# Performance work log

Measured on AMD Instinct MI355X. Metric: run time of the kernel, lower is better.

The kernel has to match this reference:

```python
import jax, jax.numpy as jnp
import numpy as np

IN_FEATURES = 1024
OUT_FEATURES = 1024
B, S = 8, 4096


def setup_inputs() -> dict:
    key = jax.random.key(0)
    kx, kw = jax.random.split(key)
    x = jax.random.normal(kx, (B, S, IN_FEATURES), dtype=jnp.float32)
    # weight initialized as randn * 0.1, shape [out_features, in_features]
    weight = jax.random.normal(kw, (OUT_FEATURES, IN_FEATURES), dtype=jnp.float32) * 0.1
    bias = jnp.zeros((OUT_FEATURES,), dtype=jnp.float32)
    return {"x": x, "weight": weight, "bias": bias}


def reference(x, weight, bias):
    # BitNetLinear eval-mode forward.
    # Weight quantization to ternary {-1, 0, +1} with mean-abs scale.
    w_scale = jnp.mean(jnp.abs(weight))  # scalar
    q_weight = jnp.sign(weight) * (jnp.abs(weight) > 0.5 * w_scale).astype(weight.dtype)
    # Activation quantization to int8 range with global abs-max scale.
    i_scale = jnp.max(jnp.abs(x)) / 127.0  # scalar
    q_input = jnp.clip(jnp.round(x / i_scale), -128.0, 127.0)
    # Float GEMM on quantized values, then dequant with both scales.
    out = jnp.einsum('bsk,ok->bso', q_input, q_weight) * w_scale * i_scale
    out = out + bias  # bias added after dequant, matching the torch code
    return out
```

## Files before the change

### kernel.cpp

```cpp
#include <hip/hip_runtime.h>
#include <stdint.h>


#define MK_M 32768
#define MK_K 1024
#define MK_N 1024

typedef __attribute__((ext_vector_type(4))) int int32x4;

#define WS_MAXP_OFF 64
#define WS_PART_OFF 8448
#define WS_QW_OFF 16384
#define WS_QX_OFF (16384 + (1 << 20))
#define WS_NEEDED (WS_QX_OFF + (size_t)MK_M * MK_K)

__global__ void kmax_x(const float4* __restrict__ x4, float* __restrict__ maxp, long n4) {
    float m = 0.f;
    long stride = (long)gridDim.x * blockDim.x;
    for (long i = (long)blockIdx.x * blockDim.x + threadIdx.x; i < n4; i += stride) {
        float4 v = x4[i];
        m = fmaxf(m, fmaxf(fmaxf(fabsf(v.x), fabsf(v.y)), fmaxf(fabsf(v.z), fabsf(v.w))));
    }
    #pragma unroll
    for (int off = 1; off < 64; off <<= 1) m = fmaxf(m, __shfl_xor(m, off));
    __shared__ float sm[4];
    int lane = threadIdx.x & 63, wid = threadIdx.x >> 6;
    if (lane == 0) sm[wid] = m;
    __syncthreads();
    if (threadIdx.x == 0) maxp[blockIdx.x] = fmaxf(fmaxf(sm[0], sm[1]), fmaxf(sm[2], sm[3]));
}

__global__ void ksum_w(const float4* __restrict__ w4, double* __restrict__ partials) {
    double s = 0.0;
    for (int i = blockIdx.x * 256 + threadIdx.x; i < (1 << 18); i += 256 * 256) {
        float4 v = w4[i];
        s += (double)fabsf(v.x);
        s += (double)fabsf(v.y);
        s += (double)fabsf(v.z);
        s += (double)fabsf(v.w);
    }
    __shared__ double sd[256];
    sd[threadIdx.x] = s;
    __syncthreads();
    for (int h = 128; h > 0; h >>= 1) {
        if ((int)threadIdx.x < h) sd[threadIdx.x] += sd[threadIdx.x + h];
        __syncthreads();
    }
    if (threadIdx.x == 0) partials[blockIdx.x] = sd[0];
}

__global__ void kfin(const double* __restrict__ partials, const float* __restrict__ maxp,
                     float* __restrict__ wscp, float* __restrict__ iscp) {
    int t = threadIdx.x;
    float m = 0.f;
    #pragma unroll
    for (int j = 0; j < 32; ++j) m = fmaxf(m, maxp[t + 64 * j]);
    double s = partials[4 * t] + partials[4 * t + 1] + partials[4 * t + 2] + partials[4 * t + 3];
    #pragma unroll
    for (int off = 1; off < 64; off <<= 1) {
        m = fmaxf(m, __shfl_xor(m, off));
        s = s + __shfl_xor(s, off);
    }
    if (t == 0) {
        *wscp = (float)(s / 1048576.0);
        *iscp = m / 127.0f;
    }
}

__global__ void kquant_w(const float4* __restrict__ w4, unsigned* __restrict__ qw,
                         const float* __restrict__ wscp) {
    float thr = 0.5f * (*wscp);
    int stride = gridDim.x * blockDim.x;
    for (int i = blockIdx.x * blockDim.x + threadIdx.x; i < (1 << 18); i += stride) {
        float4 v = w4[i];
        int q0 = (fabsf(v.x) > thr) ? (v.x > 0.f ? 1 : -1) : 0;
        int q1 = (fabsf(v.y) > thr) ? (v.y > 0.f ? 1 : -1) : 0;
        int q2 = (fabsf(v.z) > thr) ? (v.z > 0.f ? 1 : -1) : 0;
        int q3 = (fabsf(v.w) > thr) ? (v.w > 0.f ? 1 : -1) : 0;
        qw[i] = (q0 & 0xff) | ((q1 & 0xff) << 8) | ((q2 & 0xff) << 16) | ((q3 & 0xff) << 24);
    }
}

__global__ void kquant_x(const float4* __restrict__ x4, unsigned* __restrict__ qx,
                         const float* __restrict__ iscp, long n4) {
    float isc = *iscp;
    long stride = (long)gridDim.x * blockDim.x;
    for (long i = (long)blockIdx.x * blockDim.x + threadIdx.x; i < n4; i += stride) {
        float4 v = x4[i];
        float q0 = fminf(fmaxf(rintf(v.x / isc), -128.f), 127.f);
        float q1 = fminf(fmaxf(rintf(v.y / isc), -128.f), 127.f);
        float q2 = fminf(fmaxf(rintf(v.z / isc), -128.f), 127.f);
        float q3 = fminf(fmaxf(rintf(v.w / isc), -128.f), 127.f);
        int i0 = (int)q0, i1 = (int)q1, i2 = (int)q2, i3 = (int)q3;
        qx[i] = (i0 & 0xff) | ((i1 & 0xff) << 8) | ((i2 & 0xff) << 16) | ((i3 & 0xff) << 24);
    }
}

__global__ __launch_bounds__(512, 2) void kgemm(
    const char* __restrict__ qx, const char* __restrict__ qw,
    const float* __restrict__ bias, const float* __restrict__ wscp,
    const float* __restrict__ iscp, float* __restrict__ out)
{
    __shared__ __align__(16) char smem[3 * 32768];

    const int t = threadIdx.x;
    const int l = t & 63;
    const int w = t >> 6;
    const int wm = w >> 2;
    const int wn = w & 3;

    const int bid = blockIdx.x;
    const int wg = (bid & 7) * 64 + (bid >> 3);
    const int tm = wg >> 2, tn = wg & 3;
    const long m0 = (long)tm * 256;
    const int n0 = tn * 256;

    const int grow = t >> 2;
    const int gch = (t & 3) ^ ((t >> 3) & 3);
    const long goff = (long)grow * MK_K + gch * 16;
    const int loff = t * 16;

    const char* gAt = qx + m0 * MK_K + goff;
    const char* gBt = qw + (long)n0 * MK_K + goff;

    int32x4 acc[8][4];
    #pragma unroll
    for (int mi = 0; mi < 8; ++mi)
        #pragma unroll
        for (int ni = 0; ni < 4; ++ni) acc[mi][ni] = (int32x4)0;

    auto stage = [&](int u, int kt, int b) {
        char* nbase = smem + b * 32768;
        const char* src;
        char* dst;
        if (u < 2) {
            src = gAt + (long)u * 128 * MK_K + kt * 64;
            dst = nbase + u * 8192 + loff;
        } else {
            src = gBt + (long)(u - 2) * 128 * MK_K + kt * 64;
            dst = nbase + 16384 + (u - 2) * 8192 + loff;
        }
        __builtin_amdgcn_global_load_lds(
            (const __attribute__((address_space(1))) void*)src,
            (__attribute__((address_space(3))) void*)dst, 16, 0, 0);
    };

    #pragma unroll
    for (int u = 0; u < 4; ++u) stage(u, 0, 0);
    #pragma unroll
    for (int u = 0; u < 4; ++u) stage(u, 1, 1);

    for (int kt = 0; kt < 16; ++kt) {
        if (kt < 15) asm volatile("s_waitcnt vmcnt(4)" ::: "memory");
        else         asm volatile("s_waitcnt vmcnt(0)" ::: "memory");
        __builtin_amdgcn_s_barrier();

        const int cb = kt % 3;
        const int nb = (kt + 2) % 3;
        const char* bufA = smem + cb * 32768;
        const char* bufB = bufA + 16384;

        int32x4 af[8], bf[4];
        #pragma unroll
        for (int i = 0; i < 8; ++i) {
            int row = wm * 128 + i * 16 + (l & 15);
            int ch = (l >> 4) ^ ((row >> 1) & 3);
            af[i] = *(const int32x4*)(bufA + row * 64 + ch * 16);
        }
        #pragma unroll
        for (int i = 0; i < 4; ++i) {
            int row = wn * 64 + i * 16 + (l & 15);
            int ch = (l >> 4) ^ ((row >> 1) & 3);
            bf[i] = *(const int32x4*)(bufB + row * 64 + ch * 16);
        }
        if (kt < 14) {
            #pragma unroll
            for (int u = 0; u < 4; ++u) stage(u, kt + 2, nb);
        }
        __builtin_amdgcn_s_setprio(1);
        #pragma unroll
        for (int mi = 0; mi < 8; ++mi)
            #pragma unroll
            for (int ni = 0; ni < 4; ++ni)
                acc[mi][ni] = __builtin_amdgcn_mfma_i32_16x16x64_i8(
                    af[mi], bf[ni], acc[mi][ni], 0, 0, 0);
        __builtin_amdgcn_s_setprio(0);
    }

    const float wsc = *wscp, isc = *iscp;
    const int crow = (l >> 4) * 4;
    const int ccol = l & 15;
    #pragma unroll
    for (int mi = 0; mi < 8; ++mi) {
        #pragma unroll
        for (int ni = 0; ni < 4; ++ni) {
            long r0 = m0 + wm * 128 + mi * 16 + crow;
            int c = n0 + wn * 64 + ni * 16 + ccol;
            float b = bias[c];
            #pragma unroll
            for (int j = 0; j < 4; ++j) {
                out[(r0 + j) * MK_N + c] = ((float)acc[mi][ni][j] * wsc) * isc + b;
            }
        }
    }
}

extern "C" void kernel_launch(void* const* d_in, const int* in_sizes, int n_in,
                              void* d_out, int out_size, void* d_ws, size_t ws_size,
                              hipStream_t stream) {
    const float* x = (const float*)d_in[0];
    const float* wt = (const float*)d_in[1];
    const float* bias = (const float*)d_in[2];
    float* out = (float*)d_out;

    if (ws_size < WS_NEEDED) return;

    char* ws = (char*)d_ws;
    float* wscp = (float*)(ws + 0);
    float* iscp = (float*)(ws + 4);
    float* maxp = (float*)(ws + WS_MAXP_OFF);
    double* partials = (double*)(ws + WS_PART_OFF);
    char* qw = ws + WS_QW_OFF;
    char* qx = ws + WS_QX_OFF;

    const long n_x = (long)in_sizes[0];
    const long n4_x = n_x >> 2;

    kmax_x<<<2048, 256, 0, stream>>>((const float4*)x, maxp, n4_x);
    ksum_w<<<256, 256, 0, stream>>>((const float4*)wt, partials);
    kfin<<<1, 64, 0, stream>>>(partials, maxp, wscp, iscp);
    kquant_w<<<256, 256, 0, stream>>>((const float4*)wt, (unsigned*)qw, wscp);
    kquant_x<<<2048, 256, 0, stream>>>((const float4*)x, (unsigned*)qx, iscp, n4_x);

    const int grid = (MK_M / 256) * (MK_N / 256);
    kgemm<<<grid, 512, 0, stream>>>(qx, qw, bias, wscp, iscp, out);
}
```

Baseline: 109.9 us.

## Merge prep kernels and load GEMM B fragments directly from global memory

Merges the x abs-max and weight abs-sum reductions into one launch. The final reduction moves into the quantize kernels, so five pre-GEMM launches become three. The GEMM no longer stages the weight tile in LDS: each wave loads its B fragments straight from global memory into registers with inline asm, double-buffered across k-steps. The A buffer goes from triple to double buffering, which reduces LDS use. The risk is that direct global loads of B are less coalesced, rely on cache reuse across waves, and add register pressure.

```diff
diff --git a/kernel.cpp b/kernel.cpp
--- a/kernel.cpp
+++ b/kernel.cpp
@@ -14,62 +14,56 @@
 #define WS_QX_OFF (16384 + (1 << 20))
 #define WS_NEEDED (WS_QX_OFF + (size_t)MK_M * MK_K)
 
-__global__ void kmax_x(const float4* __restrict__ x4, float* __restrict__ maxp, long n4) {
-    float m = 0.f;
-    long stride = (long)gridDim.x * blockDim.x;
-    for (long i = (long)blockIdx.x * blockDim.x + threadIdx.x; i < n4; i += stride) {
-        float4 v = x4[i];
-        m = fmaxf(m, fmaxf(fmaxf(fabsf(v.x), fabsf(v.y)), fmaxf(fabsf(v.z), fabsf(v.w))));
-    }
-    #pragma unroll
-    for (int off = 1; off < 64; off <<= 1) m = fmaxf(m, __shfl_xor(m, off));
-    __shared__ float sm[4];
-    int lane = threadIdx.x & 63, wid = threadIdx.x >> 6;
-    if (lane == 0) sm[wid] = m;
+__global__ void kprep(const float4* __restrict__ x4, const float4* __restrict__ w4,
+                      float* __restrict__ maxp, double* __restrict__ partials, long n4x) {
+    const int bid = blockIdx.x;
+    if (bid < 2048) {
+        float m = 0.f;
+        const long stride = 2048L * 256;
+        for (long i = (long)bid * 256 + threadIdx.x; i < n4x; i += stride) {
+            float4 v = x4[i];
+            m = fmaxf(m, fmaxf(fmaxf(fabsf(v.x), fabsf(v.y)), fmaxf(fabsf(v.z), fabsf(v.w))));
+        }
+        #pragma unroll
+        for (int off = 1; off < 64; off <<= 1) m = fmaxf(m, __shfl_xor(m, off));
+        __shared__ float sm[4];
+        int lane = threadIdx.x & 63, wid = threadIdx.x >> 6;
+        if (lane == 0) sm[wid] = m;
+        __syncthreads();
+        if (threadIdx.x == 0) maxp[bid] = fmaxf(fmaxf(sm[0], sm[1]), fmaxf(sm[2], sm[3]));
+    } else {
+        double s = 0.0;
+        for (int i = (bid - 2048) * 256 + threadIdx.x; i < (1 << 18); i += 64 * 256) {
+            float4 v = w4[i];
+            s += (double)fabsf(v.x);
+            s += (double)fabsf(v.y);
+            s += (double)fabsf(v.z);
+            s += (double)fabsf(v.w);
+        }
+        __shared__ double sd[256];
+        sd[threadIdx.x] = s;
+        __syncthreads();
+        for (int h = 128; h > 0; h >>= 1) {
+            if ((int)threadIdx.x < h) sd[threadIdx.x] += sd[threadIdx.x + h];
+            __syncthreads();
+        }
+        if (threadIdx.x == 0) partials[bid - 2048] = sd[0];
+    }
+}
+
+__global__ void kquant_w(const float4* __restrict__ w4, unsigned* __restrict__ qw,
+                         const double* __restrict__ partials, float* __restrict__ wscp) {
+    __shared__ double sws;
+    if (threadIdx.x < 64) {
+        double s = partials[threadIdx.x];
+        #pragma unroll
+        for (int off = 1; off < 64; off <<= 1) s += __shfl_xor(s, off);
+        if (threadIdx.x == 0) sws = s;
+    }
     __syncthreads();
-    if (threadIdx.x == 0) maxp[blockIdx.x] = fmaxf(fmaxf(sm[0], sm[1]), fmaxf(sm[2], sm[3]));
-}
-
-__global__ void ksum_w(const float4* __restrict__ w4, double* __restrict__ partials) {
-    double s = 0.0;
-    for (int i = blockIdx.x * 256 + threadIdx.x; i < (1 << 18); i += 256 * 256) {
-        float4 v = w4[i];
-        s += (double)fabsf(v.x);
-        s += (double)fabsf(v.y);
-        s += (double)fabsf(v.z);
-        s += (double)fabsf(v.w);
-    }
-    __shared__ double sd[256];
-    sd[threadIdx.x] = s;
-    __syncthreads();
-    for (int h = 128; h > 0; h >>= 1) {
-        if ((int)threadIdx.x < h) sd[threadIdx.x] += sd[threadIdx.x + h];
-        __syncthreads();
-    }
-    if (threadIdx.x == 0) partials[blockIdx.x] = sd[0];
-}
-
-__global__ void kfin(const double* __restrict__ partials, const float* __restrict__ maxp,
-                     float* __restrict__ wscp, float* __restrict__ iscp) {
-    int t = threadIdx.x;
-    float m = 0.f;
-    #pragma unroll
-    for (int j = 0; j < 32; ++j) m = fmaxf(m, maxp[t + 64 * j]);
-    double s = partials[4 * t] + partials[4 * t + 1] + partials[4 * t + 2] + partials[4 * t + 3];
-    #pragma unroll
-    for (int off = 1; off < 64; off <<= 1) {
-        m = fmaxf(m, __shfl_xor(m, off));
-        s = s + __shfl_xor(s, off);
-    }
-    if (t == 0) {
-        *wscp = (float)(s / 1048576.0);
-        *iscp = m / 127.0f;
-    }
-}
-
-__global__ void kquant_w(const float4* __restrict__ w4, unsigned* __restrict__ qw,
-                         const float* __restrict__ wscp) {
-    float thr = 0.5f * (*wscp);
+    float wsc = (float)(sws / 1048576.0);
+    if (blockIdx.x == 0 && threadIdx.x == 0) *wscp = wsc;
+    float thr = 0.5f * wsc;
     int stride = gridDim.x * blockDim.x;
     for (int i = blockIdx.x * blockDim.x + threadIdx.x; i < (1 << 18); i += stride) {
         float4 v = w4[i];
@@ -82,8 +76,18 @@
 }
 
 __global__ void kquant_x(const float4* __restrict__ x4, unsigned* __restrict__ qx,
-                         const float* __restrict__ iscp, long n4) {
-    float isc = *iscp;
+                         const float* __restrict__ maxp, float* __restrict__ iscp, long n4) {
+    float m = 0.f;
+    #pragma unroll
+    for (int j = 0; j < 8; ++j) m = fmaxf(m, maxp[threadIdx.x + 256 * j]);
+    #pragma unroll
+    for (int off = 1; off < 64; off <<= 1) m = fmaxf(m, __shfl_xor(m, off));
+    __shared__ float sm[4];
+    int lane = threadIdx.x & 63, wid = threadIdx.x >> 6;
+    if (lane == 0) sm[wid] = m;
+    __syncthreads();
+    float isc = fmaxf(fmaxf(sm[0], sm[1]), fmaxf(sm[2], sm[3])) / 127.0f;
+    if (blockIdx.x == 0 && threadIdx.x == 0) *iscp = isc;
     long stride = (long)gridDim.x * blockDim.x;
     for (long i = (long)blockIdx.x * blockDim.x + threadIdx.x; i < n4; i += stride) {
         float4 v = x4[i];
@@ -101,7 +105,7 @@
     const float* __restrict__ bias, const float* __restrict__ wscp,
     const float* __restrict__ iscp, float* __restrict__ out)
 {
-    __shared__ __align__(16) char smem[3 * 32768];
+    __shared__ __align__(16) char smem[2 * 16384];
 
     const int t = threadIdx.x;
     const int l = t & 63;
@@ -116,75 +120,80 @@
     const int n0 = tn * 256;
 
     const int grow = t >> 2;
-    const int gch = (t & 3) ^ ((t >> 3) & 3);
-    const long goff = (long)grow * MK_K + gch * 16;
-    const int loff = t * 16;
-
-    const char* gAt = qx + m0 * MK_K + goff;
-    const char* gBt = qw + (long)n0 * MK_K + goff;
-
-    int32x4 acc[8][4];
-    #pragma unroll
-    for (int mi = 0; mi < 8; ++mi)
-        #pragma unroll
-        for (int ni = 0; ni < 4; ++ni) acc[mi][ni] = (int32x4)0;
-
-    auto stage = [&](int u, int kt, int b) {
-        char* nbase = smem + b * 32768;
-        const char* src;
-        char* dst;
-        if (u < 2) {
-            src = gAt + (long)u * 128 * MK_K + kt * 64;
-            dst = nbase + u * 8192 + loff;
-        } else {
-            src = gBt + (long)(u - 2) * 128 * MK_K + kt * 64;
-            dst = nbase + 16384 + (u - 2) * 8192 + loff;
-        }
+    const int gch = (t & 3) ^ ((grow >> 1) & 3);
+    const char* gAt = qx + (m0 + grow) * (long)MK_K + gch * 16;
+
+    auto stage = [&](int kt1, int b) {
+        char* dst = smem + b * 16384 + t * 16;
+        const char* src = gAt + kt1 * 64;
         __builtin_amdgcn_global_load_lds(
             (const __attribute__((address_space(1))) void*)src,
             (__attribute__((address_space(3))) void*)dst, 16, 0, 0);
+        __builtin_amdgcn_global_load_lds(
+            (const __attribute__((address_space(1))) void*)(src + 128 * (long)MK_K),
+            (__attribute__((address_space(3))) void*)(dst + 8192), 16, 0, 0);
     };
 
-    #pragma unroll
-    for (int u = 0; u < 4; ++u) stage(u, 0, 0);
-    #pragma unroll
-    for (int u = 0; u < 4; ++u) stage(u, 1, 1);
-
-    for (int kt = 0; kt < 16; ++kt) {
-        if (kt < 15) asm volatile("s_waitcnt vmcnt(4)" ::: "memory");
-        else         asm volatile("s_waitcnt vmcnt(0)" ::: "memory");
+    const unsigned vo0 = (unsigned)((n0 + wn * 64 + 0 * 16 + (l & 15)) * MK_K + (l >> 4) * 16);
+    const unsigned vo1 = vo0 + 16 * MK_K;
+    const unsigned vo2 = vo0 + 32 * MK_K;
+    const unsigned vo3 = vo0 + 48 * MK_K;
+
+    int32x4 acc[8][4];
+    #pragma unroll
+    for (int mi = 0; mi < 8; ++mi)
+        #pragma unroll
+        for (int ni = 0; ni < 4; ++ni) acc[mi][ni] = (int32x4)0;
+
+    int32x4 bfA[4], bfB[4];
+
+    stage(0, 0);
+    {
+        const char* sb = qw;
+        asm volatile("global_load_dwordx4 %0, %1, %2" : "=v"(bfA[0]) : "v"(vo0), "s"(sb));
+        asm volatile("global_load_dwordx4 %0, %1, %2" : "=v"(bfA[1]) : "v"(vo1), "s"(sb));
+        asm volatile("global_load_dwordx4 %0, %1, %2" : "=v"(bfA[2]) : "v"(vo2), "s"(sb));
+        asm volatile("global_load_dwordx4 %0, %1, %2" : "=v"(bfA[3]) : "v"(vo3), "s"(sb));
+    }
+
+    auto body = [&](int kt, int32x4 (&bfc)[4], int32x4 (&bfn)[4]) {
+        asm volatile("s_waitcnt vmcnt(4)" ::: "memory");
         __builtin_amdgcn_s_barrier();
-
-        const int cb = kt % 3;
-        const int nb = (kt + 2) % 3;
-        const char* bufA = smem + cb * 32768;
-        const char* bufB = bufA + 16384;
-
-        int32x4 af[8], bf[4];
+        __builtin_amdgcn_sched_barrier(0);
+
+        const char* bufA = smem + (kt & 1) * 16384;
+        int32x4 af[8];
         #pragma unroll
         for (int i = 0; i < 8; ++i) {
             int row = wm * 128 + i * 16 + (l & 15);
             int ch = (l >> 4) ^ ((row >> 1) & 3);
             af[i] = *(const int32x4*)(bufA + row * 64 + ch * 16);
         }
-        #pragma unroll
-        for (int i = 0; i < 4; ++i) {
-            int row = wn * 64 + i * 16 + (l & 15);
-            int ch = (l >> 4) ^ ((row >> 1) & 3);
-            bf[i] = *(const int32x4*)(bufB + row * 64 + ch * 16);
-        }
-        if (kt < 14) {
-            #pragma unroll
-            for (int u = 0; u < 4; ++u) stage(u, kt + 2, nb);
-        }
+        if (kt < 15) {
+            stage(kt + 1, (kt + 1) & 1);
+            const char* sb = qw + (kt + 1) * 64;
+            asm volatile("global_load_dwordx4 %0, %1, %2" : "=v"(bfn[0]) : "v"(vo0), "s"(sb));
+            asm volatile("global_load_dwordx4 %0, %1, %2" : "=v"(bfn[1]) : "v"(vo1), "s"(sb));
+            asm volatile("global_load_dwordx4 %0, %1, %2" : "=v"(bfn[2]) : "v"(vo2), "s"(sb));
+            asm volatile("global_load_dwordx4 %0, %1, %2" : "=v"(bfn[3]) : "v"(vo3), "s"(sb));
+            asm volatile("s_waitcnt vmcnt(6) lgkmcnt(0)" ::: "memory");
+        } else {
+            asm volatile("s_waitcnt vmcnt(0) lgkmcnt(0)" ::: "memory");
+        }
+        __builtin_amdgcn_sched_barrier(0);
         __builtin_amdgcn_s_setprio(1);
         #pragma unroll
         for (int mi = 0; mi < 8; ++mi)
             #pragma unroll
             for (int ni = 0; ni < 4; ++ni)
                 acc[mi][ni] = __builtin_amdgcn_mfma_i32_16x16x64_i8(
-                    af[mi], bf[ni], acc[mi][ni], 0, 0, 0);
+                    af[mi], bfc[ni], acc[mi][ni], 0, 0, 0);
         __builtin_amdgcn_s_setprio(0);
+    };
+
+    for (int kb = 0; kb < 8; ++kb) {
+        body(2 * kb,     bfA, bfB);
+        body(2 * kb + 1, bfB, bfA);
     }
 
     const float wsc = *wscp, isc = *iscp;
@@ -226,11 +235,9 @@
     const long n_x = (long)in_sizes[0];
     const long n4_x = n_x >> 2;
 
-    kmax_x<<<2048, 256, 0, stream>>>((const float4*)x, maxp, n4_x);
-    ksum_w<<<256, 256, 0, stream>>>((const float4*)wt, partials);
-    kfin<<<1, 64, 0, stream>>>(partials, maxp, wscp, iscp);
-    kquant_w<<<256, 256, 0, stream>>>((const float4*)wt, (unsigned*)qw, wscp);
-    kquant_x<<<2048, 256, 0, stream>>>((const float4*)x, (unsigned*)qx, iscp, n4_x);
+    kprep<<<2112, 256, 0, stream>>>((const float4*)x, (const float4*)wt, maxp, partials, n4_x);
+    kquant_w<<<256, 256, 0, stream>>>((const float4*)wt, (unsigned*)qw, partials, wscp);
+    kquant_x<<<2048, 256, 0, stream>>>((const float4*)x, (unsigned*)qx, maxp, iscp, n4_x);
 
     const int grid = (MK_M / 256) * (MK_N / 256);
     kgemm<<<grid, 512, 0, stream>>>(qx, qw, bias, wscp, iscp, out);
```

New measurement: 120.2 us. +9.4%, slower.

## Merge prep reductions into fewer launches and split GEMM k-step into two phases

Applied to the files above, without the earlier changes.

Combines the x abs-max and weight abs-sum reductions into one kernel and folds the final scale reductions into the quantize kernels, which drops two launches and the single-block finalize kernel. Each quantize block now re-reduces the partials redundantly. In the GEMM, each k-tile is split into two half-phases that interleave LDS fragment loads, global-to-LDS staging and MFMAs, with extra barriers between them. This lowers register pressure for fragments but adds synchronization per k-step.

```diff
diff --git a/kernel.cpp b/kernel.cpp
--- a/kernel.cpp
+++ b/kernel.cpp
@@ -14,62 +14,56 @@
 #define WS_QX_OFF (16384 + (1 << 20))
 #define WS_NEEDED (WS_QX_OFF + (size_t)MK_M * MK_K)
 
-__global__ void kmax_x(const float4* __restrict__ x4, float* __restrict__ maxp, long n4) {
-    float m = 0.f;
-    long stride = (long)gridDim.x * blockDim.x;
-    for (long i = (long)blockIdx.x * blockDim.x + threadIdx.x; i < n4; i += stride) {
-        float4 v = x4[i];
-        m = fmaxf(m, fmaxf(fmaxf(fabsf(v.x), fabsf(v.y)), fmaxf(fabsf(v.z), fabsf(v.w))));
-    }
-    #pragma unroll
-    for (int off = 1; off < 64; off <<= 1) m = fmaxf(m, __shfl_xor(m, off));
-    __shared__ float sm[4];
-    int lane = threadIdx.x & 63, wid = threadIdx.x >> 6;
-    if (lane == 0) sm[wid] = m;
+__global__ void kprep(const float4* __restrict__ x4, const float4* __restrict__ w4,
+                      float* __restrict__ maxp, double* __restrict__ partials, long n4x) {
+    const int bid = blockIdx.x;
+    if (bid < 2048) {
+        float m = 0.f;
+        const long stride = 2048L * 256;
+        for (long i = (long)bid * 256 + threadIdx.x; i < n4x; i += stride) {
+            float4 v = x4[i];
+            m = fmaxf(m, fmaxf(fmaxf(fabsf(v.x), fabsf(v.y)), fmaxf(fabsf(v.z), fabsf(v.w))));
+        }
+        #pragma unroll
+        for (int off = 1; off < 64; off <<= 1) m = fmaxf(m, __shfl_xor(m, off));
+        __shared__ float sm[4];
+        int lane = threadIdx.x & 63, wid = threadIdx.x >> 6;
+        if (lane == 0) sm[wid] = m;
+        __syncthreads();
+        if (threadIdx.x == 0) maxp[bid] = fmaxf(fmaxf(sm[0], sm[1]), fmaxf(sm[2], sm[3]));
+    } else {
+        double s = 0.0;
+        for (int i = (bid - 2048) * 256 + threadIdx.x; i < (1 << 18); i += 64 * 256) {
+            float4 v = w4[i];
+            s += (double)fabsf(v.x);
+            s += (double)fabsf(v.y);
+            s += (double)fabsf(v.z);
+            s += (double)fabsf(v.w);
+        }
+        __shared__ double sd[256];
+        sd[threadIdx.x] = s;
+        __syncthreads();
+        for (int h = 128; h > 0; h >>= 1) {
+            if ((int)threadIdx.x < h) sd[threadIdx.x] += sd[threadIdx.x + h];
+            __syncthreads();
+        }
+        if (threadIdx.x == 0) partials[bid - 2048] = sd[0];
+    }
+}
+
+__global__ void kquant_w(const float4* __restrict__ w4, unsigned* __restrict__ qw,
+                         const double* __restrict__ partials, float* __restrict__ wscp) {
+    __shared__ double sws;
+    if (threadIdx.x < 64) {
+        double s = partials[threadIdx.x];
+        #pragma unroll
+        for (int off = 1; off < 64; off <<= 1) s += __shfl_xor(s, off);
+        if (threadIdx.x == 0) sws = s;
+    }
     __syncthreads();
-    if (threadIdx.x == 0) maxp[blockIdx.x] = fmaxf(fmaxf(sm[0], sm[1]), fmaxf(sm[2], sm[3]));
-}
-
-__global__ void ksum_w(const float4* __restrict__ w4, double* __restrict__ partials) {
-    double s = 0.0;
-    for (int i = blockIdx.x * 256 + threadIdx.x; i < (1 << 18); i += 256 * 256) {
-        float4 v = w4[i];
-        s += (double)fabsf(v.x);
-        s += (double)fabsf(v.y);
-        s += (double)fabsf(v.z);
-        s += (double)fabsf(v.w);
-    }
-    __shared__ double sd[256];
-    sd[threadIdx.x] = s;
-    __syncthreads();
-    for (int h = 128; h > 0; h >>= 1) {
-        if ((int)threadIdx.x < h) sd[threadIdx.x] += sd[threadIdx.x + h];
-        __syncthreads();
-    }
-    if (threadIdx.x == 0) partials[blockIdx.x] = sd[0];
-}
-
-__global__ void kfin(const double* __restrict__ partials, const float* __restrict__ maxp,
-                     float* __restrict__ wscp, float* __restrict__ iscp) {
-    int t = threadIdx.x;
-    float m = 0.f;
-    #pragma unroll
-    for (int j = 0; j < 32; ++j) m = fmaxf(m, maxp[t + 64 * j]);
-    double s = partials[4 * t] + partials[4 * t + 1] + partials[4 * t + 2] + partials[4 * t + 3];
-    #pragma unroll
-    for (int off = 1; off < 64; off <<= 1) {
-        m = fmaxf(m, __shfl_xor(m, off));
-        s = s + __shfl_xor(s, off);
-    }
-    if (t == 0) {
-        *wscp = (float)(s / 1048576.0);
-        *iscp = m / 127.0f;
-    }
-}
-
-__global__ void kquant_w(const float4* __restrict__ w4, unsigned* __restrict__ qw,
-                         const float* __restrict__ wscp) {
-    float thr = 0.5f * (*wscp);
+    float wsc = (float)(sws / 1048576.0);
+    if (blockIdx.x == 0 && threadIdx.x == 0) *wscp = wsc;
+    float thr = 0.5f * wsc;
     int stride = gridDim.x * blockDim.x;
     for (int i = blockIdx.x * blockDim.x + threadIdx.x; i < (1 << 18); i += stride) {
         float4 v = w4[i];
@@ -82,8 +76,18 @@
 }
 
 __global__ void kquant_x(const float4* __restrict__ x4, unsigned* __restrict__ qx,
-                         const float* __restrict__ iscp, long n4) {
-    float isc = *iscp;
+                         const float* __restrict__ maxp, float* __restrict__ iscp, long n4) {
+    float m = 0.f;
+    #pragma unroll
+    for (int j = 0; j < 8; ++j) m = fmaxf(m, maxp[threadIdx.x + 256 * j]);
+    #pragma unroll
+    for (int off = 1; off < 64; off <<= 1) m = fmaxf(m, __shfl_xor(m, off));
+    __shared__ float sm[4];
+    int lane = threadIdx.x & 63, wid = threadIdx.x >> 6;
+    if (lane == 0) sm[wid] = m;
+    __syncthreads();
+    float isc = fmaxf(fmaxf(sm[0], sm[1]), fmaxf(sm[2], sm[3])) / 127.0f;
+    if (blockIdx.x == 0 && threadIdx.x == 0) *iscp = isc;
     long stride = (long)gridDim.x * blockDim.x;
     for (long i = (long)blockIdx.x * blockDim.x + threadIdx.x; i < n4; i += stride) {
         float4 v = x4[i];
@@ -159,32 +163,38 @@
         const int nb = (kt + 2) % 3;
         const char* bufA = smem + cb * 32768;
         const char* bufB = bufA + 16384;
-
-        int32x4 af[8], bf[4];
-        #pragma unroll
-        for (int i = 0; i < 8; ++i) {
-            int row = wm * 128 + i * 16 + (l & 15);
-            int ch = (l >> 4) ^ ((row >> 1) & 3);
-            af[i] = *(const int32x4*)(bufA + row * 64 + ch * 16);
-        }
-        #pragma unroll
-        for (int i = 0; i < 4; ++i) {
-            int row = wn * 64 + i * 16 + (l & 15);
-            int ch = (l >> 4) ^ ((row >> 1) & 3);
-            bf[i] = *(const int32x4*)(bufB + row * 64 + ch * 16);
-        }
-        if (kt < 14) {
-            #pragma unroll
-            for (int u = 0; u < 4; ++u) stage(u, kt + 2, nb);
-        }
-        __builtin_amdgcn_s_setprio(1);
-        #pragma unroll
-        for (int mi = 0; mi < 8; ++mi)
-            #pragma unroll
-            for (int ni = 0; ni < 4; ++ni)
-                acc[mi][ni] = __builtin_amdgcn_mfma_i32_16x16x64_i8(
-                    af[mi], bf[ni], acc[mi][ni], 0, 0, 0);
-        __builtin_amdgcn_s_setprio(0);
+        const bool do_stage = (kt < 14);
+
+        #pragma unroll
+        for (int ph = 0; ph < 2; ++ph) {
+            int32x4 af[4], bf[4];
+            #pragma unroll
+            for (int i = 0; i < 4; ++i) {
+                int row = wm * 128 + (ph * 4 + i) * 16 + (l & 15);
+                int ch = (l >> 4) ^ ((row >> 1) & 3);
+                af[i] = *(const int32x4*)(bufA + row * 64 + ch * 16);
+            }
+            #pragma unroll
+            for (int i = 0; i < 4; ++i) {
+                int row = wn * 64 + i * 16 + (l & 15);
+                int ch = (l >> 4) ^ ((row >> 1) & 3);
+                bf[i] = *(const int32x4*)(bufB + row * 64 + ch * 16);
+            }
+            if (do_stage) {
+                stage(ph * 2 + 0, kt + 2, nb);
+                stage(ph * 2 + 1, kt + 2, nb);
+            }
+            __builtin_amdgcn_s_barrier();
+            __builtin_amdgcn_s_setprio(1);
+            #pragma unroll
+            for (int mi = 0; mi < 4; ++mi)
+                #pragma unroll
+                for (int ni = 0; ni < 4; ++ni)
+                    acc[ph * 4 + mi][ni] = __builtin_amdgcn_mfma_i32_16x16x64_i8(
+                        af[mi], bf[ni], acc[ph * 4 + mi][ni], 0, 0, 0);
+            __builtin_amdgcn_s_setprio(0);
+            __builtin_amdgcn_s_barrier();
+        }
     }
 
     const float wsc = *wscp, isc = *iscp;
@@ -226,11 +236,9 @@
     const long n_x = (long)in_sizes[0];
     const long n4_x = n_x >> 2;
 
-    kmax_x<<<2048, 256, 0, stream>>>((const float4*)x, maxp, n4_x);
-    ksum_w<<<256, 256, 0, stream>>>((const float4*)wt, partials);
-    kfin<<<1, 64, 0, stream>>>(partials, maxp, wscp, iscp);
-    kquant_w<<<256, 256, 0, stream>>>((const float4*)wt, (unsigned*)qw, wscp);
-    kquant_x<<<2048, 256, 0, stream>>>((const float4*)x, (unsigned*)qx, iscp, n4_x);
+    kprep<<<2112, 256, 0, stream>>>((const float4*)x, (const float4*)wt, maxp, partials, n4_x);
+    kquant_w<<<256, 256, 0, stream>>>((const float4*)wt, (unsigned*)qw, partials, wscp);
+    kquant_x<<<2048, 256, 0, stream>>>((const float4*)x, (unsigned*)qx, maxp, iscp, n4_x);
 
     const int grid = (MK_M / 256) * (MK_N / 256);
     kgemm<<<grid, 512, 0, stream>>>(qx, qw, bias, wscp, iscp, out);
```

Measured after the change: 114.2 us. 1.04x slower.
